# Performance work log

Hardware: AMD Instinct MI355X
Metric: run time of the kernel (lower is better)

The kernel has to match this reference:

```python
import jax, jax.numpy as jnp
import numpy as np

N = 50000      # nodes
E = 1600000    # edges (before self loops)
F_IN = 1433    # input features (Cora)
H1, C1 = 8, 8  # layer1: heads, out channels per head
C2 = 7         # layer2: classes (heads=1, concat=False)
SLOPE = 0.2    # PyG GATConv default negative_slope


def _gat_layer(x, src, dst, W, a_src, a_dst, b, heads, out_ch, concat):
    """PyG-style GATConv (eval mode, self loops already in src/dst)."""
    n = x.shape[0]
    h = (x @ W).reshape(n, heads, out_ch)                 # [N,H,C]
    alpha_s = jnp.einsum('nhc,hc->nh', h, a_src)          # [N,H]
    alpha_d = jnp.einsum('nhc,hc->nh', h, a_dst)          # [N,H]
    e = jax.nn.leaky_relu(alpha_s[src] + alpha_d[dst], SLOPE)  # [E,H]
    # segment softmax over incoming edges per destination node
    m = jax.ops.segment_max(e, dst, num_segments=n)       # [N,H]
    ex = jnp.exp(e - m[dst])
    denom = jax.ops.segment_sum(ex, dst, num_segments=n)  # [N,H]
    alpha = ex / (denom[dst] + 1e-16)                     # [E,H]
    out = jax.ops.segment_sum(h[src] * alpha[..., None], dst, num_segments=n)  # [N,H,C]
    out = out.reshape(n, heads * out_ch) if concat else out.mean(axis=1)
    return out + b


def setup_inputs() -> dict:
    key = jax.random.key(0)
    ks = jax.random.split(key, 10)
    x = jax.random.normal(ks[0], (N, F_IN), jnp.float32)
    edge_index = jax.random.randint(ks[1], (2, E), 0, N, jnp.int32)
    s = 0.1
    return {
        'x': x,
        'edge_index': edge_index,
        'W1': jax.random.normal(ks[2], (F_IN, H1 * C1), jnp.float32) * s,
        'att_src1': jax.random.normal(ks[3], (H1, C1), jnp.float32) * s,
        'att_dst1': jax.random.normal(ks[4], (H1, C1), jnp.float32) * s,
        'b1': jnp.zeros((H1 * C1,), jnp.float32),
        'W2': jax.random.normal(ks[5], (H1 * C1, C2), jnp.float32) * s,
        'att_src2': jax.random.normal(ks[6], (1, C2), jnp.float32) * s,
        'att_dst2': jax.random.normal(ks[7], (1, C2), jnp.float32) * s,
        'b2': jnp.zeros((C2,), jnp.float32),
    }


def reference(x, edge_index, W1, att_src1, att_dst1, b1, W2, att_src2, att_dst2, b2):
    loop = jnp.arange(N, dtype=edge_index.dtype)
    src = jnp.concatenate([edge_index[0], loop])   # add_self_loops=True
    dst = jnp.concatenate([edge_index[1], loop])
    h = _gat_layer(x, src, dst, W1, att_src1, att_dst1, b1, H1, C1, True)   # [N,64]
    h = jax.nn.elu(h)
    out = _gat_layer(h, src, dst, W2, att_src2, att_dst2, b2, 1, C2, False)  # [N,7]
    return jax.nn.log_softmax(out, axis=1)
```

## Files before the change

### kernel.cpp

```cpp
#include <hip/hip_runtime.h>
#include <hip/hip_bf16.h>

static constexpr int NN      = 50000;
static constexpr int FIN     = 1433;
static constexpr int KPAD    = 1440;
static constexpr int NB_SCAN = (NN + 255) / 256;

typedef __bf16 bf16x8 __attribute__((ext_vector_type(8)));
typedef float  f32x4  __attribute__((ext_vector_type(4)));

__device__ __forceinline__ float leaky02(float v){ return v >= 0.f ? v : 0.2f * v; }
__device__ __forceinline__ float bflo(unsigned u){ return __uint_as_float(u << 16); }
__device__ __forceinline__ float bfhi(unsigned u){ return __uint_as_float(u & 0xffff0000u); }

__device__ __forceinline__ void gld_lds4(const float* g, float* l){
    __builtin_amdgcn_global_load_lds(
        (const __attribute__((address_space(1))) unsigned int*)g,
        (__attribute__((address_space(3))) unsigned int*)l, 4, 0, 0);
}

__global__ __launch_bounds__(256) void k_prep(const float* __restrict__ W1,
                                              __bf16* __restrict__ w1h, __bf16* __restrict__ w1l,
                                              int* __restrict__ deg){
    int bid = blockIdx.x;
    if (bid < 64){
        int c = bid;
        for (int k = threadIdx.x; k < KPAD; k += 256){
            float v = (k < FIN) ? W1[(size_t)k * 64 + c] : 0.f;
            __bf16 hi = (__bf16)v;
            w1h[(size_t)c * KPAD + k] = hi;
            w1l[(size_t)c * KPAD + k] = (__bf16)(v - (float)hi);
        }
    } else {
        int i = (bid - 64) * 256 + threadIdx.x;
        if (i < NN) deg[i] = 0;
    }
}

__global__ __launch_bounds__(256) void k_rank(const int* __restrict__ dst, int* __restrict__ deg,
                                              int* __restrict__ rank, int E){
    int e = blockIdx.x * 256 + threadIdx.x;
    if (e < E) rank[e] = atomicAdd(&deg[dst[e]], 1);
}

__global__ __launch_bounds__(256) void k_scan1(const int* __restrict__ deg, int* __restrict__ bsum){
    __shared__ int red[256];
    int i = blockIdx.x * 256 + threadIdx.x;
    red[threadIdx.x] = (i < NN) ? deg[i] : 0;
    __syncthreads();
    for (int off = 128; off > 0; off >>= 1){
        if (threadIdx.x < off) red[threadIdx.x] += red[threadIdx.x + off];
        __syncthreads();
    }
    if (threadIdx.x == 0) bsum[blockIdx.x] = red[0];
}

__global__ __launch_bounds__(256) void k_scan2(const int* __restrict__ bsum, int* __restrict__ bofs){
    __shared__ int s[256];
    int t = threadIdx.x;
    s[t] = (t < NB_SCAN) ? bsum[t] : 0;
    __syncthreads();
    for (int off = 1; off < 256; off <<= 1){
        int v = s[t];
        int a = (t >= off) ? s[t - off] : 0;
        __syncthreads();
        s[t] = v + a;
        __syncthreads();
    }
    if (t < NB_SCAN) bofs[t] = (t > 0) ? s[t - 1] : 0;
}

__global__ __launch_bounds__(256) void k_scan3(const int* __restrict__ deg, const int* __restrict__ bofs,
                                               int* __restrict__ row_off){
    __shared__ int s[256];
    int t = threadIdx.x;
    int i = blockIdx.x * 256 + t;
    int d = (i < NN) ? deg[i] : 0;
    s[t] = d;
    __syncthreads();
    for (int off = 1; off < 256; off <<= 1){
        int v = s[t];
        int a = (t >= off) ? s[t - off] : 0;
        __syncthreads();
        s[t] = v + a;
        __syncthreads();
    }
    int excl = s[t] - d + bofs[blockIdx.x];
    if (i < NN){
        row_off[i] = excl;
        if (i == NN - 1) row_off[NN] = excl + d;
    }
}

__global__ __launch_bounds__(256) void k_scatter(const int* __restrict__ src, const int* __restrict__ dst,
                                                 const int* __restrict__ rank, const int* __restrict__ row_off,
                                                 int* __restrict__ csr, int E){
    int e = blockIdx.x * 256 + threadIdx.x;
    if (e < E) csr[row_off[dst[e]] + rank[e]] = src[e];
}

__global__ __launch_bounds__(256, 3) void k_gemm1(const float* __restrict__ x,
    const __bf16* __restrict__ w1h, const __bf16* __restrict__ w1l,
    const float* __restrict__ a_s, const float* __restrict__ a_d,
    __bf16* __restrict__ Hb0, __bf16* __restrict__ Hb1,
    __bf16* __restrict__ asadA, __bf16* __restrict__ asadB)
{
    __shared__ float As[2 * 64 * 68];
    const int tid = threadIdx.x;
    const int w    = tid >> 6;
    const int lane = tid & 63;
    const int lr   = lane & 15;
    const int lk   = lane >> 4;
    const int rbase = blockIdx.x * 64;

    unsigned rowoff[16];
    #pragma unroll
    for (int i = 0; i < 16; ++i){
        int rg = rbase + w * 16 + i; if (rg >= NN) rg = NN - 1;
        rowoff[i] = (unsigned)rg * (unsigned)FIN + (unsigned)lane;
    }

    const __bf16* bh_p = w1h + (size_t)(w * 16 + lr) * KPAD + lk * 8;
    const __bf16* bl_p = w1l + (size_t)(w * 16 + lr) * KPAD + lk * 8;

    f32x4 acc[4] = {{0,0,0,0},{0,0,0,0},{0,0,0,0},{0,0,0,0}};

    #pragma unroll
    for (int i = 0; i < 16; ++i)
        gld_lds4(x + rowoff[i], &As[(w * 16 + i) * 68]);
    __syncthreads();

    for (int kb = 0; kb < 22; ++kb){
        const int cur = kb & 1;
        if (kb < 21){
            const float* gsrc = x + (kb + 1) * 64;
            float* lb = &As[(1 - cur) * 4352];
            #pragma unroll
            for (int i = 0; i < 16; ++i)
                gld_lds4(gsrc + rowoff[i], lb + (w * 16 + i) * 68);
        }
        const int kA = kb * 64;
        bf16x8 bh0 = *(const bf16x8*)(bh_p + kA);
        bf16x8 bl0 = *(const bf16x8*)(bl_p + kA);
        bf16x8 bh1 = *(const bf16x8*)(bh_p + kA + 32);
        bf16x8 bl1 = *(const bf16x8*)(bl_p + kA + 32);
        const float* ab = &As[cur * 4352] + lk * 8;
        #pragma unroll
        for (int ks = 0; ks < 2; ++ks){
            bf16x8 bh = ks ? bh1 : bh0;
            bf16x8 bl = ks ? bl1 : bl0;
            #pragma unroll
            for (int t = 0; t < 4; ++t){
                const float* p = ab + (t * 16 + lr) * 68 + ks * 32;
                f32x4 v0 = *(const f32x4*)p;
                f32x4 v1 = *(const f32x4*)(p + 4);
                bf16x8 ah, al;
                #pragma unroll
                for (int e = 0; e < 4; ++e){
                    __bf16 h0 = (__bf16)v0[e];
                    ah[e]     = h0; al[e]     = (__bf16)(v0[e] - (float)h0);
                    __bf16 h1 = (__bf16)v1[e];
                    ah[e + 4] = h1; al[e + 4] = (__bf16)(v1[e] - (float)h1);
                }
                acc[t] = __builtin_amdgcn_mfma_f32_16x16x32_bf16(ah, bh, acc[t], 0, 0, 0);
                acc[t] = __builtin_amdgcn_mfma_f32_16x16x32_bf16(al, bh, acc[t], 0, 0, 0);
                acc[t] = __builtin_amdgcn_mfma_f32_16x16x32_bf16(ah, bl, acc[t], 0, 0, 0);
            }
        }
        __syncthreads();
    }

    {
        bf16x8 bh = *(const bf16x8*)(bh_p + 1408);
        bf16x8 bl = *(const bf16x8*)(bl_p + 1408);
        #pragma unroll
        for (int t = 0; t < 4; ++t){
            int rg = rbase + t * 16 + lr; if (rg >= NN) rg = NN - 1;
            const float* xr = x + (size_t)rg * FIN;
            bf16x8 ah, al;
            #pragma unroll
            for (int e = 0; e < 8; ++e){
                int k = 1408 + lk * 8 + e;
                float v = (k < FIN) ? xr[k] : 0.f;
                __bf16 h = (__bf16)v;
                ah[e] = h; al[e] = (__bf16)(v - (float)h);
            }
            acc[t] = __builtin_amdgcn_mfma_f32_16x16x32_bf16(ah, bh, acc[t], 0, 0, 0);
            acc[t] = __builtin_amdgcn_mfma_f32_16x16x32_bf16(al, bh, acc[t], 0, 0, 0);
            acc[t] = __builtin_amdgcn_mfma_f32_16x16x32_bf16(ah, bl, acc[t], 0, 0, 0);
        }
    }

    __syncthreads();
    const int col = w * 16 + lr;
    __bf16* hbp = (col < 32) ? Hb0 : Hb1;
    const int cc = col & 31;
    #pragma unroll
    for (int t = 0; t < 4; ++t){
        #pragma unroll
        for (int r = 0; r < 4; ++r){
            int rib = t * 16 + lk * 4 + r;
            float v = acc[t][r];
            As[rib * 68 + col] = v;
            int row = rbase + rib;
            if (row < NN) hbp[(size_t)row * 32 + cc] = (__bf16)v;
        }
    }
    __syncthreads();
    #pragma unroll
    for (int it = 0; it < 2; ++it){
        int task = tid + it * 256;
        int row  = task >> 3;
        int hh   = task & 7;
        int grow = rbase + row;
        if (grow < NN){
            const float* hr = &As[row * 68 + hh * 8];
            float s = 0.f, dd = 0.f;
            #pragma unroll
            for (int c = 0; c < 8; ++c){
                float v = hr[c];
                s  = fmaf(v, a_s[hh * 8 + c], s);
                dd = fmaf(v, a_d[hh * 8 + c], dd);
            }
            if (hh < 4){
                asadA[(size_t)grow * 8 + hh]     = (__bf16)s;
                asadA[(size_t)grow * 8 + 4 + hh] = (__bf16)dd;
            } else {
                asadB[(size_t)grow * 8 + (hh - 4)]     = (__bf16)s;
                asadB[(size_t)grow * 8 + 4 + (hh - 4)] = (__bf16)dd;
            }
        }
    }
}

__global__ __launch_bounds__(256, 8) void k_layer1p(const __bf16* __restrict__ asadP,
    const __bf16* __restrict__ HbP, const int* __restrict__ row_off, const int* __restrict__ csr,
    const float* __restrict__ b1P, float* __restrict__ x2, int colbase)
{
    const int d  = blockIdx.x * 4 + (threadIdx.x >> 6);
    const int l  = threadIdx.x & 63;
    const int q  = l >> 4;
    const int sl = l & 15;
    const int c0 = 2 * sl;
    const int h  = sl >> 2;
    const float adv = (float)asadP[(size_t)d * 8 + 4 + h];

    float den = 0.f, a0 = 0.f, a1 = 0.f;
    if (q == 0){
        float as_d = (float)asadP[(size_t)d * 8 + h];
        float p0 = __expf(leaky02(as_d + adv) - 20.f);
        unsigned hw = *(const unsigned*)&HbP[(size_t)d * 32 + c0];
        den = p0;
        a0 = p0 * bflo(hw);
        a1 = p0 * bfhi(hw);
    }

    const int beg = row_off[d], end = row_off[d + 1];
    const int nb = (end - beg + 7) >> 3;
    int csrv = 0;
    if (nb > 0){
        int idx = beg + (l & 7); if (idx >= end) idx = end - 1;
        csrv = __builtin_nontemporal_load(csr + idx);
    }
    for (int b = 0; b < nb; ++b){
        const int base = beg + b * 8;
        int ncsr = 0;
        if (b + 1 < nb){
            int idx = base + 8 + (l & 7); if (idx >= end) idx = end - 1;
            ncsr = __builtin_nontemporal_load(csr + idx);
        }
        int s0 = __shfl(csrv, q, 8);
        int s1 = __shfl(csrv, 4 + q, 8);
        const bool v0 = (base + q) < end;
        const bool v1 = (base + 4 + q) < end;
        unsigned hw0 = 0, hw1 = 0; float av0 = 0.f, av1 = 0.f;
        if (v0){ hw0 = *(const unsigned*)&HbP[(size_t)s0 * 32 + c0];
                 av0 = (float)asadP[(size_t)s0 * 8 + h]; }
        if (v1){ hw1 = *(const unsigned*)&HbP[(size_t)s1 * 32 + c0];
                 av1 = (float)asadP[(size_t)s1 * 8 + h]; }
        if (v0){
            float p = __expf(leaky02(av0 + adv) - 20.f);
            den += p; a0 = fmaf(p, bflo(hw0), a0); a1 = fmaf(p, bfhi(hw0), a1);
        }
        if (v1){
            float p = __expf(leaky02(av1 + adv) - 20.f);
            den += p; a0 = fmaf(p, bflo(hw1), a0); a1 = fmaf(p, bfhi(hw1), a1);
        }
        csrv = ncsr;
    }

    a0  += __shfl_xor(a0, 16, 64);  a0  += __shfl_xor(a0, 32, 64);
    a1  += __shfl_xor(a1, 16, 64);  a1  += __shfl_xor(a1, 32, 64);
    den += __shfl_xor(den, 16, 64); den += __shfl_xor(den, 32, 64);

    if (q == 0){
        float o0 = a0 / den + b1P[c0];
        float o1 = a1 / den + b1P[c0 + 1];
        o0 = (o0 > 0.f) ? o0 : (__expf(o0) - 1.f);
        o1 = (o1 > 0.f) ? o1 : (__expf(o1) - 1.f);
        float2 ov = make_float2(o0, o1);
        *(float2*)&x2[(size_t)d * 64 + colbase + c0] = ov;
    }
}

__global__ __launch_bounds__(256) void k_gemm2(const float* __restrict__ x2, const float* __restrict__ W2,
    const float* __restrict__ aw_in, const float* __restrict__ dw_in,
    float* __restrict__ h2a, float* __restrict__ ad2)
{
    __shared__ float w2s[448];
    __shared__ float aw[7], dw[7];
    int tid = threadIdx.x;
    for (int i = tid; i < 448; i += 256) w2s[i] = W2[i];
    if (tid < 7){ aw[tid] = aw_in[tid]; dw[tid] = dw_in[tid]; }
    __syncthreads();
    int n = blockIdx.x * 256 + tid;
    if (n >= NN) return;
    const float4* xp = (const float4*)(x2 + (size_t)n * 64);
    float acc[7] = {0.f,0.f,0.f,0.f,0.f,0.f,0.f};
    #pragma unroll
    for (int q = 0; q < 16; ++q){
        float4 v = xp[q];
        float vv[4] = {v.x, v.y, v.z, v.w};
        #pragma unroll
        for (int u = 0; u < 4; ++u){
            int k = q * 4 + u;
            #pragma unroll
            for (int c = 0; c < 7; ++c) acc[c] = fmaf(vv[u], w2s[k * 7 + c], acc[c]);
        }
    }
    float s = 0.f, d = 0.f;
    #pragma unroll
    for (int c = 0; c < 7; ++c){ s = fmaf(acc[c], aw[c], s); d = fmaf(acc[c], dw[c], d); }
    float* hp = h2a + (size_t)n * 8;
    #pragma unroll
    for (int c = 0; c < 7; ++c) hp[c] = acc[c];
    hp[7] = s;
    ad2[n] = d;
}

__global__ __launch_bounds__(256) void k_layer2(const float* __restrict__ ad2,
    const float* __restrict__ h2a, const int* __restrict__ row_off, const int* __restrict__ csr,
    const float* __restrict__ b2, float* __restrict__ out)
{
    int tid  = threadIdx.x;
    int node = blockIdx.x * 32 + (tid >> 3);
    int c    = tid & 7;
    int lane = tid & 63;
    int gb   = lane & ~7;
    if (node >= NN) return;
    float adv   = ad2[node];
    float vself = h2a[(size_t)node * 8 + c];
    float as_n  = __shfl(vself, gb + 7, 64);
    float e0 = leaky02(as_n + adv);
    float p0 = __expf(e0 - 20.f);
    float den = p0;
    float acc = p0 * vself;
    int beg = row_off[node], end = row_off[node + 1];
    for (int base = beg; base < end; base += 16){
        int cnt = end - base; if (cnt > 16) cnt = 16;
        int j1  = 8 + c;
        int cs0 = csr[base + (c  < cnt ? c  : cnt - 1)];
        int cs1 = csr[base + (j1 < cnt ? j1 : cnt - 1)];
        float val[16];
        #pragma unroll
        for (int t = 0; t < 16; ++t){
            if (t < cnt){
                int s = (t < 8) ? __shfl(cs0, gb + t, 64) : __shfl(cs1, gb + t - 8, 64);
                val[t] = h2a[(size_t)s * 8 + c];
            }
        }
        #pragma unroll
        for (int t = 0; t < 16; ++t){
            if (t < cnt){
                float as_s = __shfl(val[t], gb + 7, 64);
                float e = leaky02(as_s + adv);
                float p = __expf(e - 20.f);
                den += p;
                acc  = fmaf(p, val[t], acc);
            }
        }
    }
    float v = (c < 7) ? (acc / den + b2[c]) : -1e30f;
    float m = v;
    m = fmaxf(m, __shfl_xor(m, 1, 64));
    m = fmaxf(m, __shfl_xor(m, 2, 64));
    m = fmaxf(m, __shfl_xor(m, 4, 64));
    float ex = (c < 7) ? __expf(v - m) : 0.f;
    float s7 = ex;
    s7 += __shfl_xor(s7, 1, 64);
    s7 += __shfl_xor(s7, 2, 64);
    s7 += __shfl_xor(s7, 4, 64);
    if (c < 7) out[(size_t)node * 7 + c] = v - m - __logf(s7);
}

extern "C" void kernel_launch(void* const* d_in, const int* in_sizes, int n_in,
                              void* d_out, int out_size, void* d_ws, size_t ws_size,
                              hipStream_t stream)
{
    (void)n_in; (void)out_size; (void)ws_size;
    const float* x      = (const float*)d_in[0];
    const int*   ei     = (const int*)d_in[1];
    const int    E      = in_sizes[1] / 2;
    const float* W1     = (const float*)d_in[2];
    const float* asrc1  = (const float*)d_in[3];
    const float* adst1  = (const float*)d_in[4];
    const float* b1     = (const float*)d_in[5];
    const float* W2     = (const float*)d_in[6];
    const float* asrc2  = (const float*)d_in[7];
    const float* adst2  = (const float*)d_in[8];
    const float* b2     = (const float*)d_in[9];
    float* out = (float*)d_out;

    char* p = (char*)d_ws;
    auto alloc = [&](size_t bytes) -> void* {
        void* r = (void*)p;
        p += (bytes + 255) & ~(size_t)255;
        return r;
    };
    int*    deg     = (int*)alloc((size_t)NN * 4);
    int*    row_off = (int*)alloc((size_t)(NN + 1) * 4);
    int*    rank    = (int*)alloc((size_t)E * 4);
    int*    bsum    = (int*)alloc((size_t)NB_SCAN * 4);
    int*    bofs    = (int*)alloc((size_t)NB_SCAN * 4);
    int*    csr     = (int*)alloc((size_t)E * 4);
    __bf16* w1h     = (__bf16*)alloc((size_t)64 * KPAD * 2);
    __bf16* w1l     = (__bf16*)alloc((size_t)64 * KPAD * 2);
    __bf16* Hb0     = (__bf16*)alloc((size_t)NN * 32 * 2);
    __bf16* Hb1     = (__bf16*)alloc((size_t)NN * 32 * 2);
    __bf16* asadA   = (__bf16*)alloc((size_t)NN * 8 * 2);
    __bf16* asadB   = (__bf16*)alloc((size_t)NN * 8 * 2);
    float*  x2      = (float*)alloc((size_t)NN * 64 * 4);
    float*  h2a     = (float*)alloc((size_t)NN * 8 * 4);
    float*  ad2     = (float*)alloc((size_t)NN * 4);

    const int* src = ei;
    const int* dst = ei + E;

    k_prep   <<<64 + NB_SCAN, 256, 0, stream>>>(W1, w1h, w1l, deg);
    k_rank   <<<(E + 255) / 256, 256, 0, stream>>>(dst, deg, rank, E);
    k_scan1  <<<NB_SCAN, 256, 0, stream>>>(deg, bsum);
    k_scan2  <<<1, 256, 0, stream>>>(bsum, bofs);
    k_scan3  <<<NB_SCAN, 256, 0, stream>>>(deg, bofs, row_off);
    k_scatter<<<(E + 255) / 256, 256, 0, stream>>>(src, dst, rank, row_off, csr, E);
    k_gemm1  <<<(NN + 63) / 64, 256, 0, stream>>>(x, w1h, w1l, asrc1, adst1,
                                                  Hb0, Hb1, asadA, asadB);
    k_layer1p<<<NN / 4, 256, 0, stream>>>(asadA, Hb0, row_off, csr, b1,      x2, 0);
    k_layer1p<<<NN / 4, 256, 0, stream>>>(asadB, Hb1, row_off, csr, b1 + 32, x2, 32);
    k_gemm2  <<<(NN + 255) / 256, 256, 0, stream>>>(x2, W2, asrc2, adst2, h2a, ad2);
    k_layer2 <<<(NN + 31) / 32, 256, 0, stream>>>(ad2, h2a, row_off, csr, b2, out);
}
```

Measured before the change: 352.9 us.

## Convert A tile to bf16 hi/lo once per block in shared memory

In the first-layer GEMM, every wave used to convert the same fp32 A tile into bf16 hi/lo pairs on its own, so the conversion ran four times per tile. Now the block converts the tile once, cooperatively, into two bf16 LDS buffers, and each wave loads ready MFMA operands from them. The fp32 staging buffer drops from double to single buffering, and the launch bound rises to 4 blocks per CU. This trades less redundant ALU work for an extra barrier each iteration and less overlap between the prefetch and the conversion.

```diff
diff --git a/kernel.cpp b/kernel.cpp
--- a/kernel.cpp
+++ b/kernel.cpp
@@ -99,19 +99,23 @@
     if (e < E) csr[row_off[dst[e]] + rank[e]] = src[e];
 }
 
-__global__ __launch_bounds__(256, 3) void k_gemm1(const float* __restrict__ x,
+__global__ __launch_bounds__(256, 4) void k_gemm1(const float* __restrict__ x,
     const __bf16* __restrict__ w1h, const __bf16* __restrict__ w1l,
     const float* __restrict__ a_s, const float* __restrict__ a_d,
     __bf16* __restrict__ Hb0, __bf16* __restrict__ Hb1,
     __bf16* __restrict__ asadA, __bf16* __restrict__ asadB)
 {
-    __shared__ float As[2 * 64 * 68];
-    const int tid = threadIdx.x;
+    __shared__ float  As[64 * 68];
+    __shared__ __bf16 AH[64 * 72];
+    __shared__ __bf16 AL[64 * 72];
+    const int tid  = threadIdx.x;
     const int w    = tid >> 6;
     const int lane = tid & 63;
     const int lr   = lane & 15;
     const int lk   = lane >> 4;
     const int rbase = blockIdx.x * 64;
+    const int cr = tid >> 2;
+    const int cg = (tid & 3) * 16;
 
     unsigned rowoff[16];
     #pragma unroll
@@ -131,37 +135,54 @@
     __syncthreads();
 
     for (int kb = 0; kb < 22; ++kb){
-        const int cur = kb & 1;
+        {
+            const float* rp = &As[cr * 68 + cg];
+            f32x4 v[4];
+            #pragma unroll
+            for (int j = 0; j < 4; ++j) v[j] = *(const f32x4*)(rp + j * 4);
+            bf16x8 hv0, hv1, lv0, lv1;
+            #pragma unroll
+            for (int j = 0; j < 2; ++j){
+                #pragma unroll
+                for (int e = 0; e < 4; ++e){
+                    float a0 = v[2 * j][e], a1 = v[2 * j + 1][e];
+                    __bf16 h0 = (__bf16)a0, h1 = (__bf16)a1;
+                    if (j == 0){ hv0[e] = h0; hv0[e + 4] = h1;
+                                 lv0[e] = (__bf16)(a0 - (float)h0);
+                                 lv0[e + 4] = (__bf16)(a1 - (float)h1); }
+                    else       { hv1[e] = h0; hv1[e + 4] = h1;
+                                 lv1[e] = (__bf16)(a0 - (float)h0);
+                                 lv1[e + 4] = (__bf16)(a1 - (float)h1); }
+                }
+            }
+            *(bf16x8*)&AH[cr * 72 + cg]     = hv0;
+            *(bf16x8*)&AH[cr * 72 + cg + 8] = hv1;
+            *(bf16x8*)&AL[cr * 72 + cg]     = lv0;
+            *(bf16x8*)&AL[cr * 72 + cg + 8] = lv1;
+        }
+        __syncthreads();
+
         if (kb < 21){
             const float* gsrc = x + (kb + 1) * 64;
-            float* lb = &As[(1 - cur) * 4352];
             #pragma unroll
             for (int i = 0; i < 16; ++i)
-                gld_lds4(gsrc + rowoff[i], lb + (w * 16 + i) * 68);
-        }
+                gld_lds4(gsrc + rowoff[i], &As[(w * 16 + i) * 68]);
+        }
+
         const int kA = kb * 64;
         bf16x8 bh0 = *(const bf16x8*)(bh_p + kA);
         bf16x8 bl0 = *(const bf16x8*)(bl_p + kA);
         bf16x8 bh1 = *(const bf16x8*)(bh_p + kA + 32);
         bf16x8 bl1 = *(const bf16x8*)(bl_p + kA + 32);
-        const float* ab = &As[cur * 4352] + lk * 8;
         #pragma unroll
         for (int ks = 0; ks < 2; ++ks){
             bf16x8 bh = ks ? bh1 : bh0;
             bf16x8 bl = ks ? bl1 : bl0;
             #pragma unroll
             for (int t = 0; t < 4; ++t){
-                const float* p = ab + (t * 16 + lr) * 68 + ks * 32;
-                f32x4 v0 = *(const f32x4*)p;
-                f32x4 v1 = *(const f32x4*)(p + 4);
-                bf16x8 ah, al;
-                #pragma unroll
-                for (int e = 0; e < 4; ++e){
-                    __bf16 h0 = (__bf16)v0[e];
-                    ah[e]     = h0; al[e]     = (__bf16)(v0[e] - (float)h0);
-                    __bf16 h1 = (__bf16)v1[e];
-                    ah[e + 4] = h1; al[e + 4] = (__bf16)(v1[e] - (float)h1);
-                }
+                const int ao = (t * 16 + lr) * 72 + ks * 32 + lk * 8;
+                bf16x8 ah = *(const bf16x8*)&AH[ao];
+                bf16x8 al = *(const bf16x8*)&AL[ao];
                 acc[t] = __builtin_amdgcn_mfma_f32_16x16x32_bf16(ah, bh, acc[t], 0, 0, 0);
                 acc[t] = __builtin_amdgcn_mfma_f32_16x16x32_bf16(al, bh, acc[t], 0, 0, 0);
                 acc[t] = __builtin_amdgcn_mfma_f32_16x16x32_bf16(ah, bl, acc[t], 0, 0, 0);
```

New measurement: 351.3 us. About the same (-0.5%).
